# Performance work log

Hardware: AMD Instinct MI355X
Metric: run time of the kernel (lower is better)

Reference implementation:

```python
import jax, jax.numpy as jnp
import numpy as np

T, N, D, E, O = 2, 4096, 1024, 8, 1024

def setup_inputs() -> dict:
    key = jax.random.key(0)
    k1, k2, k3 = jax.random.split(key, 3)
    x = jax.random.normal(k1, (T, N, D), dtype=jnp.float32)
    Wg = jax.random.normal(k2, (T, D, E), dtype=jnp.float32) * (1.0 / np.sqrt(D))
    We = jax.random.normal(k3, (E, D, O), dtype=jnp.float32) * (1.0 / np.sqrt(D))
    return {"x": x, "Wg": Wg, "We": We, "k": 2}


def reference(x, Wg, We, k):
    # Per-task gating logits: [T, N, E]
    logits = jnp.einsum('tnd,tde->tne', x, Wg)
    # Top-k mask per token (scatter 1.0 at top-k indices)
    _, topk_idx = jax.lax.top_k(logits, k)                      # [T, N, k]
    mask = jax.nn.one_hot(topk_idx, E, dtype=logits.dtype).sum(-2)  # [T, N, E]
    masked = mask * logits
    gates = masked / (masked.sum(-1, keepdims=True) + 1e-9)     # [T, N, E]
    # Dense expert outputs (each expert is Linear(D, O)): [T, N, E, O]
    eout = jnp.einsum('tnd,edo->tneo', x, We)
    # Weighted combine over selected experts
    out = jnp.einsum('tne,tneo->tno', gates, eout)              # [T, N, O]
    return out
```

## Files before the change

kernel.cpp:

```cpp
#include <hip/hip_runtime.h>
#include <hip/hip_bf16.h>
#include <stdint.h>

#define T_ 2
#define N_ 4096
#define D_ 1024
#define E_ 8
#define O_ 1024

#define BM 128
#define BN 128
#define BK 32

typedef __attribute__((ext_vector_type(8))) short short8;
typedef __attribute__((ext_vector_type(4))) float f32x4;

#define AS1 __attribute__((address_space(1)))
#define AS3 __attribute__((address_space(3)))

__device__ inline void gld16(const unsigned short* g, unsigned short* l) {
    __builtin_amdgcn_global_load_lds((const AS1 unsigned int*)g,
                                     (AS3 unsigned int*)l, 16, 0, 0);
}

__device__ inline unsigned short f2bf(float f) {
    union { float f; unsigned u; } v; v.f = f;
    unsigned r = v.u + 0x7fff + ((v.u >> 16) & 1);
    return (unsigned short)(r >> 16);
}

__global__ __launch_bounds__(256) void prep_kernel(
    const float* __restrict__ x, const float* __restrict__ Wg,
    const float* __restrict__ We,
    unsigned short* __restrict__ xb, unsigned short* __restrict__ Wbp,
    int* __restrict__ route, float2* __restrict__ gpair)
{
    __shared__ __align__(16) char smem[E_ * D_ * 4];
    int tid = threadIdx.x;

    if (blockIdx.x < 1024) {
        float (*WgT)[D_] = (float(*)[D_])smem;
        int wave = tid >> 6, lane = tid & 63;
        int token0 = blockIdx.x * 8;
        int t = token0 >> 12;
        const float* wgb = Wg + (size_t)t * D_ * E_;

#pragma unroll
        for (int r = 0; r < 8; ++r) {
            int f = r * 1024 + tid * 4;
            float4 v = *(const float4*)(wgb + f);
            WgT[f & 7][f >> 3]             = v.x;
            WgT[(f + 1) & 7][(f + 1) >> 3] = v.y;
            WgT[(f + 2) & 7][(f + 2) >> 3] = v.z;
            WgT[(f + 3) & 7][(f + 3) >> 3] = v.w;
        }
        __syncthreads();

#pragma unroll
        for (int tl = 0; tl < 2; ++tl) {
            int token = token0 + wave * 2 + tl;
            const float* xrow = x + (size_t)token * D_;

            float4 xv[4];
#pragma unroll
            for (int c = 0; c < 4; ++c)
                xv[c] = *(const float4*)(xrow + c * 256 + lane * 4);

            float acc[E_] = {0.f, 0.f, 0.f, 0.f, 0.f, 0.f, 0.f, 0.f};
#pragma unroll
            for (int c = 0; c < 4; ++c) {
                int d0 = c * 256 + lane * 4;
                unsigned lo = f2bf(xv[c].x) | ((unsigned)f2bf(xv[c].y) << 16);
                unsigned hi = f2bf(xv[c].z) | ((unsigned)f2bf(xv[c].w) << 16);
                *(uint2*)(&xb[(size_t)token * D_ + d0]) = make_uint2(lo, hi);
#pragma unroll
                for (int e = 0; e < E_; ++e) {
                    float4 w = *(const float4*)(&WgT[e][d0]);
                    acc[e] += xv[c].x * w.x + xv[c].y * w.y + xv[c].z * w.z + xv[c].w * w.w;
                }
            }
#pragma unroll
            for (int off = 1; off < 64; off <<= 1) {
#pragma unroll
                for (int e = 0; e < E_; ++e) acc[e] += __shfl_xor(acc[e], off, 64);
            }

            if (lane == 0) {
                float best = acc[0]; int bi = 0;
#pragma unroll
                for (int e = 1; e < E_; ++e) if (acc[e] > best) { best = acc[e]; bi = e; }
                float sec = -INFINITY; int si = 0;
#pragma unroll
                for (int e = 0; e < E_; ++e) if (e != bi && acc[e] > sec) { sec = acc[e]; si = e; }
                float s = best + sec + 1e-9f;
                route[token] = bi | (si << 8);
                gpair[token] = make_float2(best / s, sec / s);
            }
        }
    } else {
        unsigned short* P = (unsigned short*)smem;

        int b = blockIdx.x - 1024;
        int e  = b >> 7;
        int oy = (b & 127) >> 3;
        int dz = b & 7;
        int o0 = oy * 64, d0 = dz * 128;

#pragma unroll
        for (int r = 0; r < 32; ++r) {
            int lin = r * 256 + tid;
            int dd = lin >> 6, oo = lin & 63;
            P[oo * 136 + dd] = f2bf(We[((size_t)(e * D_ + d0 + dd)) * O_ + o0 + oo]);
        }
        __syncthreads();

#pragma unroll
        for (int w = 0; w < 4; ++w) {
            int ci = w * 256 + tid;
            int oo = ci >> 4, dc = ci & 15;
            uint4 v = *(const uint4*)&P[oo * 136 + dc * 8];
            int o = o0 + oo;
            int ot = o >> 7, nn = o & 127;
            unsigned short* dst =
                Wbp + ((size_t)((e * 8 + ot) * 128 + nn)) * D_ + d0 + dc * 8;
            *(uint4*)dst = v;
        }
    }
}

__global__ __launch_bounds__(1024) void build_lists(
    const int* __restrict__ route, const float2* __restrict__ gpair,
    int* __restrict__ toklist, float* __restrict__ gatelist,
    int* __restrict__ counts)
{
    int g = blockIdx.x;
    int t = g >> 3, e = g & 7;
    int tid = threadIdx.x;
    int wave = tid >> 6, lane = tid & 63;

    __shared__ int waveSum[16];
    __shared__ int base;
    if (tid == 0) base = 0;

    for (int c = 0; c < N_; c += 1024) {
        int n = c + tid;
        int r = route[t * N_ + n];
        int e0 = r & 255, e1 = (r >> 8) & 255;
        bool sel = (e0 == e) || (e1 == e);
        unsigned long long b = __ballot(sel);
        int pre  = __popcll(b & ((1ull << lane) - 1ull));
        if (lane == 0) waveSum[wave] = __popcll(b);
        __syncthreads();
        int woff = 0, total = 0;
#pragma unroll
        for (int w = 0; w < 16; ++w) {
            int s = waveSum[w];
            total += s;
            woff += (w < wave) ? s : 0;
        }
        if (sel) {
            int p = base + woff + pre;
            int slot = (e0 == e) ? 0 : 1;
            toklist[g * N_ + p] = n | (slot << 16);
            float2 gp = gpair[t * N_ + n];
            gatelist[g * N_ + p] = (e0 == e) ? gp.x : gp.y;
        }
        __syncthreads();
        if (tid == 0) base += total;
    }
    __syncthreads();
    if (tid == 0) counts[g] = base;
}

__global__ __launch_bounds__(512, 4) void moe_gemm(
    const unsigned short* __restrict__ xb,
    const unsigned short* __restrict__ Wbp,
    const int* __restrict__ toklist, const float* __restrict__ gatelist,
    const int* __restrict__ counts, float* __restrict__ out)
{
    int lin = blockIdx.x;
    int mt  = lin >> 7;
    int u   = lin & 127;
    int xcd = u & 7;
    int v   = u >> 3;
    int g   = 2 * xcd + (v >> 3);
    int ot  = v & 7;
    int t   = g >> 3;

    int cnt = counts[g];
    int m0 = mt * BM;
    if (m0 >= cnt) return;

    __shared__ __align__(16) unsigned short As[2][BM * BK];
    __shared__ __align__(16) unsigned short Bs[2][BN * BK];
    __shared__ int   tokS[BM];
    __shared__ float gateS[BM];

    int tid = threadIdx.x;
    if (tid < BM) {
        int r = m0 + tid;
        tokS[tid]  = (r < cnt) ? toklist[g * N_ + r]  : -1;
        gateS[tid] = (r < cnt) ? gatelist[g * N_ + r] : 0.f;
    }
    __syncthreads();

    int wave = tid >> 6, lane = tid & 63;
    int lr = lane >> 2;
    int sg = (lane & 3) ^ ((lane >> 3) & 3);
    int ar = wave * 16 + lr;
    int tok = max(tokS[ar], 0) & 0xFFFF;
    const unsigned short* ag = xb + ((size_t)(t * N_ + tok)) * D_ + sg * 8;
    const unsigned short* wb = Wbp + ((size_t)((g & 7) * 8 + ot) * 128) * D_;
    const unsigned short* bg = wb + (size_t)ar * D_ + sg * 8;

    int fr = lane & 15, q = lane >> 4;
    int wm = (wave & 1) * 64;
    int wn = (wave >> 1) * 32;
    int fp = (q ^ ((fr >> 1) & 3)) * 8;

    f32x4 acc[4][2];
#pragma unroll
    for (int mi = 0; mi < 4; ++mi)
#pragma unroll
        for (int ni = 0; ni < 2; ++ni) acc[mi][ni] = (f32x4){0.f, 0.f, 0.f, 0.f};

    gld16(ag, &As[0][wave * 512]);
    gld16(bg, &Bs[0][wave * 512]);

#define KSTEP(CUR, NXT, IT)                                                    \
    {                                                                          \
        __syncthreads();   \
        int k1 = ((IT) + 1) * BK;                                              \
        if (k1 < D_) {                                                         \
            gld16(ag + k1, &As[NXT][wave * 512]);                              \
            gld16(bg + k1, &Bs[NXT][wave * 512]);                              \
        }                                                                      \
        short8 af[4], bf[2];                                                   \
        _Pragma("unroll") for (int mi = 0; mi < 4; ++mi)                       \
            af[mi] = *(const short8*)(&As[CUR][(wm + mi * 16 + fr) * BK + fp]);\
        _Pragma("unroll") for (int ni = 0; ni < 2; ++ni)                       \
            bf[ni] = *(const short8*)(&Bs[CUR][(wn + ni * 16 + fr) * BK + fp]);\
        _Pragma("unroll") for (int mi = 0; mi < 4; ++mi)                       \
            _Pragma("unroll") for (int ni = 0; ni < 2; ++ni)                   \
                acc[mi][ni] = __builtin_amdgcn_mfma_f32_16x16x32_bf16(         \
                    af[mi], bf[ni], acc[mi][ni], 0, 0, 0);                     \
    }

    for (int it = 0; it < D_ / BK; it += 2) {
        KSTEP(0, 1, it)
        KSTEP(1, 0, it + 1)
    }
#undef KSTEP

    float* outb = out + (size_t)t * N_ * O_;
    int ncol = ot * 128 + wn + fr;
#pragma unroll
    for (int mi = 0; mi < 4; ++mi) {
#pragma unroll
        for (int r = 0; r < 4; ++r) {
            int ml = wm + mi * 16 + q * 4 + r;
            int ent = tokS[ml];
            if (ent >= 0) {
                int tokk = ent & 0xFFFF;
                int slot = ent >> 16;
                float gate = gateS[ml];
#pragma unroll
                for (int ni = 0; ni < 2; ++ni) {
                    unsigned short* p =
                        (unsigned short*)(outb + (size_t)tokk * O_ + ncol + ni * 16);
                    p[slot] = f2bf(gate * acc[mi][ni][r]);
                }
            }
        }
    }
}

__global__ __launch_bounds__(256) void combine_kernel(float* __restrict__ out)
{
    size_t i = ((size_t)blockIdx.x * 256 + threadIdx.x) * 4;
    unsigned* po = (unsigned*)out;
    uint4 v = *(uint4*)(po + i);
    float4 r;
    union { unsigned u; float f; } a, b;
#define CMB(comp, src) a.u = (src) << 16; b.u = (src) & 0xFFFF0000u; comp = a.f + b.f
    CMB(r.x, v.x); CMB(r.y, v.y); CMB(r.z, v.z); CMB(r.w, v.w);
#undef CMB
    *(float4*)(out + i) = r;
}

extern "C" void kernel_launch(void* const* d_in, const int* in_sizes, int n_in,
                              void* d_out, int out_size, void* d_ws, size_t ws_size,
                              hipStream_t stream)
{
    const float* x  = (const float*)d_in[0];
    const float* Wg = (const float*)d_in[1];
    const float* We = (const float*)d_in[2];
    float* out = (float*)d_out;

    char* ws = (char*)d_ws;
    unsigned short* xb   = (unsigned short*)(ws);
    unsigned short* Wbp  = (unsigned short*)(ws + 16777216);
    int*   toklist       = (int*)  (ws + 33554432);
    float* gatelist      = (float*)(ws + 33816576);
    int*   counts        = (int*)  (ws + 34078720);
    int*   route         = (int*)  (ws + 34078976);
    float2* gpair        = (float2*)(ws + 34111744);

    prep_kernel<<<2048, 256, 0, stream>>>(x, Wg, We, xb, Wbp, route, gpair);
    build_lists<<<T_ * E_, 1024, 0, stream>>>(route, gpair, toklist, gatelist, counts);
    moe_gemm<<<(N_ / BM) * 8 * (T_ * E_), 512, 0, stream>>>(
        xb, Wbp, toklist, gatelist, counts, out);
    combine_kernel<<<((size_t)T_ * N_ * O_) / (256 * 4), 256, 0, stream>>>(out);
}
```

Measured before the change: 183.5 us.

## Pre-swizzle expert weights into MFMA fragment order and load B directly to registers

The weight-prep kernel now writes expert weights in a layout where each wave's 64 lanes read contiguous 16-byte MFMA B fragments per K-step. The grouped GEMM drops the B shared-memory tile and loads B fragments straight from global memory into registers, double-buffered across K steps, with an explicit vmcnt wait plus barrier in place of __syncthreads. This removes LDS traffic and LDS capacity for B and may raise occupancy. The cost is more redundant global and L2 reads of B across waves, plus reliance on the hand-placed waitcnt being correct.

Measured after the change: 177.5 us. 3.3% less time.

```diff
diff --git a/kernel.cpp b/kernel.cpp
--- a/kernel.cpp
+++ b/kernel.cpp
@@ -116,14 +116,17 @@
 
 #pragma unroll
         for (int w = 0; w < 4; ++w) {
-            int ci = w * 256 + tid;
-            int oo = ci >> 4, dc = ci & 15;
-            uint4 v = *(const uint4*)&P[oo * 136 + dc * 8];
-            int o = o0 + oo;
-            int ot = o >> 7, nn = o & 127;
-            unsigned short* dst =
-                Wbp + ((size_t)((e * 8 + ot) * 128 + nn)) * D_ + d0 + dc * 8;
-            *(uint4*)dst = v;
+            int ci   = w * 256 + tid;
+            int lane = ci & 63;
+            int c16  = (ci >> 6) & 3;
+            int ks   = ci >> 8;
+            int fr = lane & 15, q = lane >> 4;
+            uint4 v = *(const uint4*)&P[(c16 * 16 + fr) * 136 + ks * 32 + q * 8];
+            int ot  = oy >> 1;
+            int cb  = (oy * 4 + c16) & 7;
+            int ksa = dz * 4 + ks;
+            size_t idx = ((((size_t)(e * 8 + ot) * 32 + ksa) * 8 + cb) * 64 + lane) * 8;
+            *(uint4*)(Wbp + idx) = v;
         }
     }
 }
@@ -192,7 +195,6 @@
     if (m0 >= cnt) return;
 
     __shared__ __align__(16) unsigned short As[2][BM * BK];
-    __shared__ __align__(16) unsigned short Bs[2][BN * BK];
     __shared__ int   tokS[BM];
     __shared__ float gateS[BM];
 
@@ -210,8 +212,12 @@
     int ar = wave * 16 + lr;
     int tok = max(tokS[ar], 0) & 0xFFFF;
     const unsigned short* ag = xb + ((size_t)(t * N_ + tok)) * D_ + sg * 8;
-    const unsigned short* wb = Wbp + ((size_t)((g & 7) * 8 + ot) * 128) * D_;
-    const unsigned short* bg = wb + (size_t)ar * D_ + sg * 8;
+
+    const unsigned short* wf =
+        Wbp + ((size_t)((g & 7) * 8 + ot) * 32) * 4096;
+    int cb0 = (wave >> 1) * 2;
+    const unsigned short* bp0 = wf + cb0 * 512 + lane * 8;
+    const unsigned short* bp1 = bp0 + 512;
 
     int fr = lane & 15, q = lane >> 4;
     int wm = (wave & 1) * 64;
@@ -224,31 +230,39 @@
 #pragma unroll
         for (int ni = 0; ni < 2; ++ni) acc[mi][ni] = (f32x4){0.f, 0.f, 0.f, 0.f};
 
+    short8 bf0[2], bf1[2];
+
     gld16(ag, &As[0][wave * 512]);
-    gld16(bg, &Bs[0][wave * 512]);
-
-#define KSTEP(CUR, NXT, IT)                                                    \
+    asm volatile("" ::: "memory");
+    bf0[0] = *(const short8*)(bp0);
+    bf0[1] = *(const short8*)(bp1);
+
+#define KSTEP(CUR, NXT, BC, BNX, IT)                                           \
     {                                                                          \
-        __syncthreads();   \
-        int k1 = ((IT) + 1) * BK;                                              \
-        if (k1 < D_) {                                                         \
-            gld16(ag + k1, &As[NXT][wave * 512]);                              \
-            gld16(bg + k1, &Bs[NXT][wave * 512]);                              \
+        asm volatile("s_waitcnt vmcnt(2)" ::: "memory");     \
+        __builtin_amdgcn_s_barrier();                                          \
+        asm volatile("" ::: "memory");       \
+        int kk = (IT) + 1;                                                     \
+        if (kk < D_ / BK) {                                                    \
+            gld16(ag + (size_t)kk * BK, &As[NXT][wave * 512]);                 \
+            asm volatile("" ::: "memory");     \
+            BNX[0] = *(const short8*)(bp0 + (size_t)kk * 4096);                \
+            BNX[1] = *(const short8*)(bp1 + (size_t)kk * 4096);                \
         }                                                                      \
-        short8 af[4], bf[2];                                                   \
+        short8 af[4];                                                          \
         _Pragma("unroll") for (int mi = 0; mi < 4; ++mi)                       \
             af[mi] = *(const short8*)(&As[CUR][(wm + mi * 16 + fr) * BK + fp]);\
-        _Pragma("unroll") for (int ni = 0; ni < 2; ++ni)                       \
-            bf[ni] = *(const short8*)(&Bs[CUR][(wn + ni * 16 + fr) * BK + fp]);\
-        _Pragma("unroll") for (int mi = 0; mi < 4; ++mi)                       \
-            _Pragma("unroll") for (int ni = 0; ni < 2; ++ni)                   \
-                acc[mi][ni] = __builtin_amdgcn_mfma_f32_16x16x32_bf16(         \
-                    af[mi], bf[ni], acc[mi][ni], 0, 0, 0);                     \
+        _Pragma("unroll") for (int mi = 0; mi < 4; ++mi) {                     \
+            acc[mi][0] = __builtin_amdgcn_mfma_f32_16x16x32_bf16(              \
+                af[mi], BC[0], acc[mi][0], 0, 0, 0);                           \
+            acc[mi][1] = __builtin_amdgcn_mfma_f32_16x16x32_bf16(              \
+                af[mi], BC[1], acc[mi][1], 0, 0, 0);                           \
+        }                                                                      \
     }
 
     for (int it = 0; it < D_ / BK; it += 2) {
-        KSTEP(0, 1, it)
-        KSTEP(1, 0, it + 1)
+        KSTEP(0, 1, bf0, bf1, it)
+        KSTEP(1, 0, bf1, bf0, it + 1)
     }
 #undef KSTEP
 
```
